# Performance work log

Hardware: AMD Instinct MI355X
Metric: run time of the kernel (lower is better)

The kernel has to match this reference:

```python
import jax, jax.numpy as jnp
from jax import lax
import numpy as np

# dims
N_DIA, DLEN = 48, 64            # 48 dialogues, 64 utterances each
N = N_DIA * DLEN                # total utterances = 3072
D = 512                         # n_dim (modal feature dim)
H = 512                         # nhidden
NL = 2                          # GCNII layers
NS = 2                          # n_speakers
ALPHA, LAMDA = 0.1, 0.5
PI = float(np.pi)
SCALE = 0.99999                 # acos clamp factor from original code


def setup_inputs() -> dict:
    key = jax.random.key(0)
    ks = jax.random.split(key, 8)
    a = jax.random.normal(ks[0], (N, D), jnp.float32)
    v = jax.random.normal(ks[1], (N, D), jnp.float32)
    l = jax.random.normal(ks[2], (N, D), jnp.float32)
    qmask = jax.random.uniform(ks[3], (DLEN, N_DIA, NS), jnp.float32)
    dia_len = np.full((N_DIA,), DLEN, dtype=np.int64)  # static segment lengths
    # learned params
    W_spk = 0.02 * jax.random.normal(ks[4], (NS, D), jnp.float32)      # speaker_embeddings
    W0 = jax.random.normal(ks[5], (D, H), jnp.float32) / np.sqrt(D)    # graph_net.fcs[0]
    b0 = jnp.zeros((H,), jnp.float32)
    Wg = jax.random.normal(ks[6], (NL, H, H), jnp.float32) / np.sqrt(H)  # GCNII conv weights
    return {"a": a, "v": v, "l": l, "qmask": qmask, "dia_len": dia_len,
            "W_spk": W_spk, "W0": W0, "b0": b0, "Wg": Wg}


def _angular_sim(cs):
    # 1 - acos(cs*0.99999)/pi, clipped for numerical safety of acos
    return 1.0 - jnp.arccos(jnp.clip(cs * SCALE, -SCALE, SCALE)) / PI


def _build_adj(feats, seg_mask):
    # feats: list of 3 arrays [N, D]; seg_mask: [N, N] same-dialogue block mask
    n = feats[0].shape[0]
    normed = [f * jax.lax.rsqrt(jnp.sum(f * f, axis=1, keepdims=True)) for f in feats]
    adj = jnp.zeros((3 * n, 3 * n), feats[0].dtype)
    ar = jnp.arange(n)
    for m in range(3):
        for nn_ in range(3):
            if m == nn_:
                # within-modality: block-diagonal (per dialogue) angular cosine similarity
                sim = _angular_sim(normed[m] @ normed[m].T) * seg_mask
                adj = adj.at[m * n:(m + 1) * n, nn_ * n:(nn_ + 1) * n].set(sim)
            else:
                # cross-modality: only diagonal (same utterance) entries
                cs = jnp.sum(normed[m] * normed[nn_], axis=1)
                adj = adj.at[m * n + ar, nn_ * n + ar].set(_angular_sim(cs))
    # symmetric degree normalization D^-1/2 A D^-1/2
    dinv = jax.lax.rsqrt(adj.sum(axis=1))
    return adj * dinv[:, None] * dinv[None, :]


def reference(a, v, l, qmask, dia_len, W_spk, W0, b0, Wg):
    dl = np.asarray(dia_len)
    nb = dl.shape[0]
    # node -> (position-in-dialogue, dialogue-id), static from dia_len
    dia_id = np.repeat(np.arange(nb), dl)
    pos = np.concatenate([np.arange(x) for x in dl])
    qflat = qmask[pos, dia_id]                 # [N, NS], matches torch.cat order
    spk_idx = jnp.argmax(qflat, axis=-1)       # [N]
    l = l + W_spk[spk_idx]                     # use_speaker=True, 'l' in modals

    seg = jnp.asarray(dia_id)
    seg_mask = (seg[:, None] == seg[None, :]).astype(a.dtype)  # [N, N]
    adj = _build_adj([a, v, l], seg_mask)      # [3N, 3N]

    x = jnp.concatenate([a, v, l], axis=0)     # [3N, D]
    # GCNII_lyc (eval mode: dropout is identity)
    h0 = jax.nn.relu(x @ W0 + b0)              # [3N, H]
    thetas = jnp.log(LAMDA / jnp.arange(1, NL + 1, dtype=x.dtype) + 1.0)

    def step(h, wt):
        W, theta = wt
        hi = adj @ h
        support = (1.0 - ALPHA) * hi + ALPHA * h0   # variant=False
        h = jax.nn.relu(theta * (support @ W) + (1.0 - theta) * support)
        return h, None

    h, _ = lax.scan(step, h0, (Wg, thetas))
    feat = jnp.concatenate([x, h], axis=-1)    # use_residue=True -> [3N, D+H]
    n = a.shape[0]
    # regroup per-utterance modal features: [N, 3*(D+H)]
    out = jnp.concatenate([feat[:n], feat[n:2 * n], feat[2 * n:3 * n]], axis=-1)
    return out
```

## Files before the change

kernel.cpp:

```cpp
#include <hip/hip_runtime.h>
#include <math.h>

#define N_DIA 48
#define NTOT  3072
#define DD    512
#define M3    9216
#define SEG   ((size_t)NTOT * DD)

#define SCALE_F 0.99999f
#define PI_F    3.14159274101257324f

typedef __attribute__((ext_vector_type(8))) short frag8;
typedef __attribute__((ext_vector_type(4))) float f32x4;

__device__ __forceinline__ float ang_sim(float cs) {
    float cc = cs * SCALE_F;
    cc = fminf(fmaxf(cc, -SCALE_F), SCALE_F);
    return 1.0f - acosf(cc) / PI_F;
}
__device__ __forceinline__ unsigned short f2bf(float x) {
    union { float f; unsigned int u; } c; c.f = x;
    unsigned int r = c.u + 0x7fffu + ((c.u >> 16) & 1u);
    return (unsigned short)(r >> 16);
}
__device__ __forceinline__ float bf2f(unsigned short h) {
    union { unsigned int u; float f; } c; c.u = ((unsigned int)h) << 16;
    return c.f;
}
__device__ __forceinline__ void gload16(const unsigned short* g, unsigned short* s) {
    __builtin_amdgcn_global_load_lds(
        (const __attribute__((address_space(1))) unsigned int*)g,
        (__attribute__((address_space(3))) unsigned int*)s, 16, 0, 0);
}

__global__ __launch_bounds__(256) void k_pre_wt(
    const float* __restrict__ a, const float* __restrict__ v,
    const float* __restrict__ l, const float* __restrict__ qmask,
    const float* __restrict__ Wspk, const float* __restrict__ W0,
    const float* __restrict__ Wg,
    float* __restrict__ out, unsigned short* __restrict__ xb,
    float* __restrict__ invn, float* __restrict__ cross,
    unsigned short* __restrict__ Wt)
{
    __shared__ float tile[32][33];
    int b = blockIdx.x;
    if (b < 768) {
        int wv = threadIdx.x >> 6, t = threadIdx.x & 63;
        int i = b * 4 + wv;
        int pos = i & 63, dia = i >> 6;
        int qb = (pos * N_DIA + dia) * 2;
        float q0 = qmask[qb], q1 = qmask[qb + 1];
        int spk = (q0 >= q1) ? 0 : 1;
        const float4* av4 = (const float4*)(a + (size_t)i * DD);
        const float4* vv4 = (const float4*)(v + (size_t)i * DD);
        const float4* lv4 = (const float4*)(l + (size_t)i * DD);
        const float4* wv4 = (const float4*)(Wspk + (size_t)spk * DD);
        float* ob = out + (size_t)i * 3072;
        float saa = 0, svv = 0, sll = 0, sav = 0, sal = 0, svl = 0;
#pragma unroll
        for (int e = 0; e < 2; e++) {
            int idx = e * 64 + t;
            float4 xa = av4[idx], xv = vv4[idx], xd = lv4[idx], xw = wv4[idx];
            float4 xL = make_float4(xd.x + xw.x, xd.y + xw.y, xd.z + xw.z, xd.w + xw.w);
            *(float4*)(ob + idx * 4)        = xa;
            *(float4*)(ob + 1024 + idx * 4) = xv;
            *(float4*)(ob + 2048 + idx * 4) = xL;
            ushort4 ya, yv, yl;
            ya.x = f2bf(xa.x); ya.y = f2bf(xa.y); ya.z = f2bf(xa.z); ya.w = f2bf(xa.w);
            yv.x = f2bf(xv.x); yv.y = f2bf(xv.y); yv.z = f2bf(xv.z); yv.w = f2bf(xv.w);
            yl.x = f2bf(xL.x); yl.y = f2bf(xL.y); yl.z = f2bf(xL.z); yl.w = f2bf(xL.w);
            *(ushort4*)(xb + (size_t)i * DD + idx * 4) = ya;
            *(ushort4*)(xb + SEG + (size_t)i * DD + idx * 4) = yv;
            *(ushort4*)(xb + 2 * SEG + (size_t)i * DD + idx * 4) = yl;
            saa += xa.x * xa.x + xa.y * xa.y + xa.z * xa.z + xa.w * xa.w;
            svv += xv.x * xv.x + xv.y * xv.y + xv.z * xv.z + xv.w * xv.w;
            sll += xL.x * xL.x + xL.y * xL.y + xL.z * xL.z + xL.w * xL.w;
            sav += xa.x * xv.x + xa.y * xv.y + xa.z * xv.z + xa.w * xv.w;
            sal += xa.x * xL.x + xa.y * xL.y + xa.z * xL.z + xa.w * xL.w;
            svl += xv.x * xL.x + xv.y * xL.y + xv.z * xL.z + xv.w * xL.w;
        }
#pragma unroll
        for (int off = 32; off; off >>= 1) {
            saa += __shfl_down(saa, off, 64);
            svv += __shfl_down(svv, off, 64);
            sll += __shfl_down(sll, off, 64);
            sav += __shfl_down(sav, off, 64);
            sal += __shfl_down(sal, off, 64);
            svl += __shfl_down(svl, off, 64);
        }
        if (t == 0) {
            float ina = 1.0f / sqrtf(saa);
            float inv_ = 1.0f / sqrtf(svv);
            float inl = 1.0f / sqrtf(sll);
            invn[i] = ina; invn[NTOT + i] = inv_; invn[2 * NTOT + i] = inl;
            cross[i]            = ang_sim(sav * ina * inv_);
            cross[NTOT + i]     = ang_sim(sal * ina * inl);
            cross[2 * NTOT + i] = ang_sim(svl * inv_ * inl);
        }
    } else {
        int idx = b - 768;
        int mm = idx >> 8;
        int by = (idx >> 4) & 15, bx = idx & 15;
        const float* W = (mm == 0) ? W0 : Wg + (size_t)(mm - 1) * DD * DD;
        int t = threadIdx.x, tx = t & 31, ty = t >> 5;
#pragma unroll
        for (int q = 0; q < 4; q++) {
            int k = by * 32 + ty + q * 8;
            tile[ty + q * 8][tx] = W[(size_t)k * DD + bx * 32 + tx];
        }
        __syncthreads();
#pragma unroll
        for (int q = 0; q < 4; q++) {
            int n = bx * 32 + ty + q * 8;
            Wt[(size_t)mm * DD * DD + (size_t)n * DD + by * 32 + tx] = f2bf(tile[tx][ty + q * 8]);
        }
    }
}

__global__ __launch_bounds__(256) void k_gram_mfma(
    const unsigned short* __restrict__ xb, const float* __restrict__ invn,
    const float* __restrict__ cross, float* __restrict__ blk,
    float* __restrict__ dinv)
{
    __shared__ __align__(16) unsigned short Xs[16 * 2048];
    int d = blockIdx.x, m = blockIdx.y;
    int t = threadIdx.x;
    int lane = t & 63, wv = t >> 6;
    int mrow = m * NTOT + d * 64;
    const unsigned short* src = xb + (size_t)mrow * DD;
    int sunit = ((t & 3) ^ ((t >> 2) & 3)) * 8;
#pragma unroll
    for (int c = 0; c < 16; c++) {
        gload16(src + (size_t)(t >> 2) * DD + c * 32 + sunit,
                &Xs[c * 2048 + wv * 512]);
    }
    __syncthreads();

    int rsel = lane & 15, quad = lane >> 4;
    int sq = (quad ^ (rsel & 3)) * 8;
    f32x4 acc[4];
#pragma unroll
    for (int j = 0; j < 4; j++) acc[j] = (f32x4){0.f, 0.f, 0.f, 0.f};
#pragma unroll
    for (int c = 0; c < 16; c++) {
        const unsigned short* base = &Xs[c * 2048];
        frag8 bf[4];
#pragma unroll
        for (int j = 0; j < 4; j++)
            bf[j] = *(const frag8*)&base[(j * 16 + rsel) * 32 + sq];
        frag8 af = *(const frag8*)&base[(wv * 16 + rsel) * 32 + sq];
#pragma unroll
        for (int j = 0; j < 4; j++)
            acc[j] = __builtin_amdgcn_mfma_f32_16x16x32_bf16(af, bf[j], acc[j], 0, 0, 0);
    }

    size_t bbase = (size_t)(m * N_DIA + d) * 4096;
    int rowl0 = wv * 16 + quad * 4;
    float ir[4], rs[4] = {0.f, 0.f, 0.f, 0.f};
#pragma unroll
    for (int r = 0; r < 4; r++) ir[r] = invn[mrow + rowl0 + r];
#pragma unroll
    for (int j = 0; j < 4; j++) {
        int coll = j * 16 + rsel;
        float ic = invn[mrow + coll];
#pragma unroll
        for (int r = 0; r < 4; r++) {
            float sim = ang_sim(acc[j][r] * ir[r] * ic);
            blk[bbase + (size_t)(rowl0 + r) * 64 + coll] = sim;
            rs[r] += sim;
        }
    }
#pragma unroll
    for (int off = 8; off; off >>= 1)
#pragma unroll
        for (int r = 0; r < 4; r++) rs[r] += __shfl_down(rs[r], off, 16);
    if (rsel == 0) {
#pragma unroll
        for (int r = 0; r < 4; r++) {
            int gi = d * 64 + rowl0 + r;
            float c1, c2;
            if (m == 0)      { c1 = cross[gi];        c2 = cross[NTOT + gi]; }
            else if (m == 1) { c1 = cross[gi];        c2 = cross[2 * NTOT + gi]; }
            else             { c1 = cross[NTOT + gi]; c2 = cross[2 * NTOT + gi]; }
            dinv[m * NTOT + gi] = 1.0f / sqrtf(rs[r] + c1 + c2);
        }
    }
}

__global__ __launch_bounds__(256) void k_gemm(
    const unsigned short* __restrict__ A, const unsigned short* __restrict__ W,
    const float* __restrict__ bias,
    unsigned short* __restrict__ oRows, unsigned short* __restrict__ oT,
    float theta, int mode,
    const unsigned short* __restrict__ A2, unsigned short* __restrict__ oRows2)
{
    __shared__ __align__(16) char smem[53248];
    unsigned short* const As0 = (unsigned short*)smem;
    unsigned short* const As1 = (unsigned short*)(smem + 4096);
    unsigned short* const Bs0 = (unsigned short*)(smem + 8192);
    unsigned short* const Bs1 = (unsigned short*)(smem + 16384);
    unsigned short* const tH  = (unsigned short*)smem;
    unsigned short* const tR  = (unsigned short*)(smem + 17408);
    unsigned short* const tT  = (unsigned short*)(smem + 34816);

    int t = threadIdx.x, lane = t & 63, wv = t >> 6;
    int bx = blockIdx.x, by = blockIdx.y;
    const unsigned short* Ap = A;
    unsigned short* oR = oRows;
    unsigned short* oTp = oT;
    if (by >= 144) { Ap = A2; oR = oRows2; oTp = nullptr; by -= 144; }
    int mbase = by * 64, nbase = bx * 128;
    int srow = lane >> 2;
    int scol = (((lane & 3) ^ (srow & 3)) * 8);
    int rsel = lane & 15, quad = lane >> 4;
    int sq = (quad ^ (rsel & 3)) * 8;

    const unsigned short* Ag  = Ap + (size_t)(mbase + wv * 16 + srow) * DD + scol;
    const unsigned short* Bg0 = W  + (size_t)(nbase + wv * 32 + srow) * DD + scol;
    const unsigned short* Bg1 = W  + (size_t)(nbase + wv * 32 + 16 + srow) * DD + scol;

    f32x4 acc[8];
#pragma unroll
    for (int i = 0; i < 8; i++) acc[i] = (f32x4){0.f, 0.f, 0.f, 0.f};

    gload16(Ag,  As0 + wv * 512);
    gload16(Bg0, Bs0 + wv * 1024);
    gload16(Bg1, Bs0 + wv * 1024 + 512);

#pragma unroll
    for (int kt = 0; kt < 16; kt++) {
        __syncthreads();
        const unsigned short* Ac = (kt & 1) ? As1 : As0;
        const unsigned short* Bc = (kt & 1) ? Bs1 : Bs0;
        if (kt < 15) {
            unsigned short* An = (kt & 1) ? As0 : As1;
            unsigned short* Bn = (kt & 1) ? Bs0 : Bs1;
            gload16(Ag + (kt + 1) * 32,  An + wv * 512);
            gload16(Bg0 + (kt + 1) * 32, Bn + wv * 1024);
            gload16(Bg1 + (kt + 1) * 32, Bn + wv * 1024 + 512);
        }
        frag8 af[4], bfr[2];
#pragma unroll
        for (int i = 0; i < 4; i++)
            af[i] = *(const frag8*)&Ac[(i * 16 + rsel) * 32 + sq];
#pragma unroll
        for (int j = 0; j < 2; j++)
            bfr[j] = *(const frag8*)&Bc[(wv * 32 + j * 16 + rsel) * 32 + sq];
#pragma unroll
        for (int i = 0; i < 4; i++)
#pragma unroll
            for (int j = 0; j < 2; j++)
                acc[i * 2 + j] = __builtin_amdgcn_mfma_f32_16x16x32_bf16(
                    af[i], bfr[j], acc[i * 2 + j], 0, 0, 0);
    }
    __syncthreads();

    int r = t >> 2, c0 = (t & 3) * 32;
    if (mode == 1) {
        const unsigned short* srcA = Ap + (size_t)(mbase + r) * DD + nbase + c0;
#pragma unroll
        for (int u = 0; u < 4; u++)
            *(uint4*)&tH[r * 136 + c0 + u * 8] = *(const uint4*)(srcA + u * 8);
        __syncthreads();
    }
    float omt = 1.0f - theta;
#pragma unroll
    for (int i = 0; i < 4; i++)
#pragma unroll
        for (int j = 0; j < 2; j++) {
            int cl = wv * 32 + j * 16 + rsel;
            float bv = 0.f;
            if (mode == 0) bv = bias[nbase + cl];
            float vv[4];
#pragma unroll
            for (int rr = 0; rr < 4; rr++) {
                int rl = i * 16 + quad * 4 + rr;
                float x = acc[i * 2 + j][rr];
                if (mode == 0) x = fmaxf(x + bv, 0.f);
                else           x = theta * x + omt * bf2f(tH[rl * 136 + cl]);
                vv[rr] = x;
            }
#pragma unroll
            for (int rr = 0; rr < 4; rr++)
                tR[(i * 16 + quad * 4 + rr) * 136 + cl] = f2bf(vv[rr]);
            if (oTp) {
                ushort4 w4;
                w4.x = f2bf(vv[0]); w4.y = f2bf(vv[1]);
                w4.z = f2bf(vv[2]); w4.w = f2bf(vv[3]);
                *(ushort4*)&tT[cl * 72 + i * 16 + quad * 4] = w4;
            }
        }
    __syncthreads();
    {
        unsigned short* dst = oR + (size_t)(mbase + r) * DD + nbase + c0;
#pragma unroll
        for (int u = 0; u < 4; u++)
            *(uint4*)(dst + u * 8) = *(const uint4*)&tR[r * 136 + c0 + u * 8];
    }
    if (oTp) {
        int c = t >> 1, r0 = (t & 1) * 32;
        unsigned short* dst = oTp + (size_t)(nbase + c) * M3 + mbase + r0;
#pragma unroll
        for (int u = 0; u < 4; u++)
            *(uint4*)(dst + u * 8) = *(const uint4*)&tT[c * 72 + r0 + u * 8];
    }
}

__global__ __launch_bounds__(256) void k_adj(
    const float* __restrict__ blk, const float* __restrict__ cross,
    const float* __restrict__ dinv,
    const unsigned short* __restrict__ GT, const unsigned short* __restrict__ Gr,
    const unsigned short* __restrict__ P0,
// ... 93 lines not shown
        }
    }
    if (!final_mode) {
        __syncthreads();
        int r = t >> 2, c0 = (t & 3) * 32;
        unsigned short* dst = hout + (size_t)(m * NTOT + dbase + r) * DD + cbase + c0;
#pragma unroll
        for (int u = 0; u < 4; u++)
            *(uint4*)(dst + u * 8) = *(const uint4*)&OT[r * 136 + c0 + u * 8];
    }
}

extern "C" void kernel_launch(void* const* d_in, const int* in_sizes, int n_in,
                              void* d_out, int out_size, void* d_ws, size_t ws_size,
                              hipStream_t stream) {
    (void)in_sizes; (void)n_in; (void)out_size; (void)ws_size;
    const float* a     = (const float*)d_in[0];
    const float* v     = (const float*)d_in[1];
    const float* l     = (const float*)d_in[2];
    const float* qmask = (const float*)d_in[3];
    const float* Wspk  = (const float*)d_in[5];
    const float* W0    = (const float*)d_in[6];
    const float* b0    = (const float*)d_in[7];
    const float* Wg    = (const float*)d_in[8];
    float* out = (float*)d_out;
    float* ws = (float*)d_ws;

    float* invn  = ws;
    float* blk   = invn + M3;
    float* cross = blk + (size_t)3 * N_DIA * 4096;
    float* dinvp = cross + M3;
    unsigned short* Wt  = (unsigned short*)(dinvp + M3);
    unsigned short* xb  = Wt + (size_t)3 * DD * DD;
    unsigned short* h0  = xb  + 3 * SEG;
    unsigned short* G1r = h0  + 3 * SEG;
    unsigned short* G1T = G1r + 3 * SEG;
    unsigned short* h1  = G1T + 3 * SEG;
    unsigned short* G2r = xb;
    unsigned short* G2T = G1r;
    unsigned short* P02 = G1T;

    const float th1 = 0.40546510810816438f;
    const float th2 = 0.22314355131420976f;

    k_pre_wt<<<1536, 256, 0, stream>>>(a, v, l, qmask, Wspk, W0, Wg, out, xb, invn, cross, Wt);
    k_gram_mfma<<<dim3(N_DIA, 3), 256, 0, stream>>>(xb, invn, cross, blk, dinvp);

    k_gemm<<<dim3(4, 144), 256, 0, stream>>>(xb, Wt, b0, h0, nullptr, 0.f, 0, nullptr, nullptr);
    k_gemm<<<dim3(4, 144), 256, 0, stream>>>(h0, Wt + (size_t)DD * DD, nullptr, G1r, G1T,
                                             th1, 1, nullptr, nullptr);
    k_adj<<<dim3(4, N_DIA, 3), 256, 0, stream>>>(blk, cross, dinvp, G1T, G1r, G1r,
                                                 h1, nullptr, 0);
    k_gemm<<<dim3(4, 288), 256, 0, stream>>>(h1, Wt + (size_t)2 * DD * DD, nullptr, G2r, G2T,
                                             th2, 1, h0, P02);
    k_adj<<<dim3(4, N_DIA, 3), 256, 0, stream>>>(blk, cross, dinvp, G2T, G2r, P02,
                                                 nullptr, out, 1);
}
```

Before: 199.7 us.

## Fuse preprocessing with gram kernel and chain h0, G1, P02 GEMMs in one kernel

```diff
diff --git a/kernel.cpp b/kernel.cpp
--- a/kernel.cpp
+++ b/kernel.cpp
@@ -32,53 +32,86 @@
         (const __attribute__((address_space(1))) unsigned int*)g,
         (__attribute__((address_space(3))) unsigned int*)s, 16, 0, 0);
 }
-
-__global__ __launch_bounds__(256) void k_pre_wt(
+__device__ __forceinline__ float d8(float4 x0, float4 x1, float4 y0, float4 y1) {
+    return x0.x*y0.x + x0.y*y0.y + x0.z*y0.z + x0.w*y0.w
+         + x1.x*y1.x + x1.y*y1.y + x1.z*y1.z + x1.w*y1.w;
+}
+
+__global__ __launch_bounds__(512) void k_pre_gram_wt(
     const float* __restrict__ a, const float* __restrict__ v,
     const float* __restrict__ l, const float* __restrict__ qmask,
     const float* __restrict__ Wspk, const float* __restrict__ W0,
     const float* __restrict__ Wg,
     float* __restrict__ out, unsigned short* __restrict__ xb,
-    float* __restrict__ invn, float* __restrict__ cross,
-    unsigned short* __restrict__ Wt)
+    float* __restrict__ cross, float* __restrict__ blk,
+    float* __restrict__ dinv, unsigned short* __restrict__ Wt)
 {
-    __shared__ float tile[32][33];
+    __shared__ __align__(16) char smem[66816];
     int b = blockIdx.x;
-    if (b < 768) {
-        int wv = threadIdx.x >> 6, t = threadIdx.x & 63;
-        int i = b * 4 + wv;
-        int pos = i & 63, dia = i >> 6;
-        int qb = (pos * N_DIA + dia) * 2;
+    int t = threadIdx.x;
+
+    if (b >= 144) {
+        float (*tile)[32][33] = (float (*)[32][33])smem;
+        int sub = t >> 8, tid = t & 255;
+        int idx = (b - 144) * 2 + sub;
+        int mm = idx >> 8, rem = idx & 255;
+        int by = rem >> 4, bx = rem & 15;
+        const float* W = (mm == 0) ? W0 : Wg + (size_t)(mm - 1) * DD * DD;
+        int tx = tid & 31, ty = tid >> 5;
+#pragma unroll
+        for (int q = 0; q < 4; q++) {
+            int k = by * 32 + ty + q * 8;
+            tile[sub][ty + q * 8][tx] = W[(size_t)k * DD + bx * 32 + tx];
+        }
+        __syncthreads();
+#pragma unroll
+        for (int q = 0; q < 4; q++) {
+            int n = bx * 32 + ty + q * 8;
+            Wt[(size_t)mm * DD * DD + (size_t)n * DD + by * 32 + tx] = f2bf(tile[sub][tx][ty + q * 8]);
+        }
+        return;
+    }
+
+    unsigned short* Xs = (unsigned short*)smem;
+    float* invnL = (float*)(smem + 65536);
+    float* c1L = invnL + 64;
+    float* c2L = c1L + 64;
+    int d = b % N_DIA, m = b / N_DIA;
+    int lane = t & 63, wv = t >> 6;
+    int dbase = d * 64;
+
+    for (int u = 0; u < 8; u++) {
+        int r = u * 8 + wv;
+        int i = dbase + r;
+        int qb = (r * N_DIA + d) * 2;
         float q0 = qmask[qb], q1 = qmask[qb + 1];
         int spk = (q0 >= q1) ? 0 : 1;
-        const float4* av4 = (const float4*)(a + (size_t)i * DD);
-        const float4* vv4 = (const float4*)(v + (size_t)i * DD);
-        const float4* lv4 = (const float4*)(l + (size_t)i * DD);
-        const float4* wv4 = (const float4*)(Wspk + (size_t)spk * DD);
-        float* ob = out + (size_t)i * 3072;
-        float saa = 0, svv = 0, sll = 0, sav = 0, sal = 0, svl = 0;
-#pragma unroll
-        for (int e = 0; e < 2; e++) {
-            int idx = e * 64 + t;
-            float4 xa = av4[idx], xv = vv4[idx], xd = lv4[idx], xw = wv4[idx];
-            float4 xL = make_float4(xd.x + xw.x, xd.y + xw.y, xd.z + xw.z, xd.w + xw.w);
-            *(float4*)(ob + idx * 4)        = xa;
-            *(float4*)(ob + 1024 + idx * 4) = xv;
-            *(float4*)(ob + 2048 + idx * 4) = xL;
-            ushort4 ya, yv, yl;
-            ya.x = f2bf(xa.x); ya.y = f2bf(xa.y); ya.z = f2bf(xa.z); ya.w = f2bf(xa.w);
-            yv.x = f2bf(xv.x); yv.y = f2bf(xv.y); yv.z = f2bf(xv.z); yv.w = f2bf(xv.w);
-            yl.x = f2bf(xL.x); yl.y = f2bf(xL.y); yl.z = f2bf(xL.z); yl.w = f2bf(xL.w);
-            *(ushort4*)(xb + (size_t)i * DD + idx * 4) = ya;
-            *(ushort4*)(xb + SEG + (size_t)i * DD + idx * 4) = yv;
-            *(ushort4*)(xb + 2 * SEG + (size_t)i * DD + idx * 4) = yl;
-            saa += xa.x * xa.x + xa.y * xa.y + xa.z * xa.z + xa.w * xa.w;
-            svv += xv.x * xv.x + xv.y * xv.y + xv.z * xv.z + xv.w * xv.w;
-            sll += xL.x * xL.x + xL.y * xL.y + xL.z * xL.z + xL.w * xL.w;
-            sav += xa.x * xv.x + xa.y * xv.y + xa.z * xv.z + xa.w * xv.w;
-            sal += xa.x * xL.x + xa.y * xL.y + xa.z * xL.z + xa.w * xL.w;
-            svl += xv.x * xL.x + xv.y * xL.y + xv.z * xL.z + xv.w * xL.w;
-        }
+        const float4* ap = (const float4*)(a + (size_t)i * DD) + lane * 2;
+        const float4* vp = (const float4*)(v + (size_t)i * DD) + lane * 2;
+        const float4* lp = (const float4*)(l + (size_t)i * DD) + lane * 2;
+        const float4* wp = (const float4*)(Wspk + (size_t)spk * DD) + lane * 2;
+        float4 a0 = ap[0], a1 = ap[1];
+        float4 v0 = vp[0], v1 = vp[1];
+        float4 l0 = lp[0], l1 = lp[1];
+        float4 w0 = wp[0], w1 = wp[1];
+        float4 L0 = make_float4(l0.x + w0.x, l0.y + w0.y, l0.z + w0.z, l0.w + w0.w);
+        float4 L1 = make_float4(l1.x + w1.x, l1.y + w1.y, l1.z + w1.z, l1.w + w1.w);
+        float* ob = out + (size_t)i * 3072 + m * 1024 + lane * 8;
+        if (m == 0)      { *(float4*)ob = a0; *(float4*)(ob + 4) = a1; }
+        else if (m == 1) { *(float4*)ob = v0; *(float4*)(ob + 4) = v1; }
+        else             { *(float4*)ob = L0; *(float4*)(ob + 4) = L1; }
+        float4 m0, m1;
+        if (m == 0) { m0 = a0; m1 = a1; } else if (m == 1) { m0 = v0; m1 = v1; }
+        else { m0 = L0; m1 = L1; }
+        ushort4 y0, y1;
+        y0.x = f2bf(m0.x); y0.y = f2bf(m0.y); y0.z = f2bf(m0.z); y0.w = f2bf(m0.w);
+        y1.x = f2bf(m1.x); y1.y = f2bf(m1.y); y1.z = f2bf(m1.z); y1.w = f2bf(m1.w);
+        unsigned short* xg = xb + (size_t)m * SEG + (size_t)i * DD + lane * 8;
+        *(ushort4*)xg = y0; *(ushort4*)(xg + 4) = y1;
+        unsigned short* xd = &Xs[(lane >> 2) * 2048 + r * 32 + (((lane & 3) ^ (r & 3)) << 3)];
+        *(ushort4*)xd = y0; *(ushort4*)(xd + 4) = y1;
+        float saa = d8(a0, a1, a0, a1), svv = d8(v0, v1, v0, v1), sll = d8(L0, L1, L0, L1);
+        float sav = d8(a0, a1, v0, v1), sal = d8(a0, a1, L0, L1), svl = d8(v0, v1, L0, L1);
 #pragma unroll
         for (int off = 32; off; off >>= 1) {
             saa += __shfl_down(saa, off, 64);
@@ -88,103 +121,289 @@
             sal += __shfl_down(sal, off, 64);
             svl += __shfl_down(svl, off, 64);
         }
-        if (t == 0) {
+        if (lane == 0) {
             float ina = 1.0f / sqrtf(saa);
             float inv_ = 1.0f / sqrtf(svv);
             float inl = 1.0f / sqrtf(sll);
-            invn[i] = ina; invn[NTOT + i] = inv_; invn[2 * NTOT + i] = inl;
-            cross[i]            = ang_sim(sav * ina * inv_);
-            cross[NTOT + i]     = ang_sim(sal * ina * inl);
-            cross[2 * NTOT + i] = ang_sim(svl * inv_ * inl);
-        }
-    } else {
-        int idx = b - 768;
-        int mm = idx >> 8;
-        int by = (idx >> 4) & 15, bx = idx & 15;
-        const float* W = (mm == 0) ? W0 : Wg + (size_t)(mm - 1) * DD * DD;
-        int t = threadIdx.x, tx = t & 31, ty = t >> 5;
-#pragma unroll
-        for (int q = 0; q < 4; q++) {
-            int k = by * 32 + ty + q * 8;
-            tile[ty + q * 8][tx] = W[(size_t)k * DD + bx * 32 + tx];
-        }
-        __syncthreads();
-#pragma unroll
-        for (int q = 0; q < 4; q++) {
-            int n = bx * 32 + ty + q * 8;
-            Wt[(size_t)mm * DD * DD + (size_t)n * DD + by * 32 + tx] = f2bf(tile[tx][ty + q * 8]);
-        }
-    }
-}
-
-__global__ __launch_bounds__(256) void k_gram_mfma(
-    const unsigned short* __restrict__ xb, const float* __restrict__ invn,
-    const float* __restrict__ cross, float* __restrict__ blk,
-    float* __restrict__ dinv)
+            float s_av = ang_sim(sav * ina * inv_);
+            float s_al = ang_sim(sal * ina * inl);
+            float s_vl = ang_sim(svl * inv_ * inl);
+            if (m == 0) { cross[i] = s_av; cross[NTOT + i] = s_al; cross[2 * NTOT + i] = s_vl; }
+            invnL[r] = (m == 0) ? ina : ((m == 1) ? inv_ : inl);
+            c1L[r] = (m == 2) ? s_al : s_av;
+            c2L[r] = (m == 0) ? s_al : s_vl;
+        }
+    }
+    __syncthreads();
+
+    if (wv < 4) {
+        int rsel = lane & 15, quad = lane >> 4;
+        int sq = (quad ^ (rsel & 3)) * 8;
+        f32x4 acc[4];
+#pragma unroll
+        for (int j = 0; j < 4; j++) acc[j] = (f32x4){0.f, 0.f, 0.f, 0.f};
+#pragma unroll
+        for (int c = 0; c < 16; c++) {
+            const unsigned short* base = &Xs[c * 2048];
+            frag8 bf[4];
+#pragma unroll
+            for (int j = 0; j < 4; j++)
+                bf[j] = *(const frag8*)&base[(j * 16 + rsel) * 32 + sq];
+            frag8 af = *(const frag8*)&base[(wv * 16 + rsel) * 32 + sq];
+#pragma unroll
+            for (int j = 0; j < 4; j++)
+                acc[j] = __builtin_amdgcn_mfma_f32_16x16x32_bf16(af, bf[j], acc[j], 0, 0, 0);
+        }
+        size_t bbase = (size_t)(m * N_DIA + d) * 4096;
+        int rowl0 = wv * 16 + quad * 4;
+        float ir[4], rs[4] = {0.f, 0.f, 0.f, 0.f};
+#pragma unroll
+        for (int r = 0; r < 4; r++) ir[r] = invnL[rowl0 + r];
+#pragma unroll
+        for (int j = 0; j < 4; j++) {
+            int coll = j * 16 + rsel;
+            float ic = invnL[coll];
+#pragma unroll
+            for (int r = 0; r < 4; r++) {
+                float sim = ang_sim(acc[j][r] * ir[r] * ic);
+                blk[bbase + (size_t)(rowl0 + r) * 64 + coll] = sim;
+                rs[r] += sim;
+            }
+        }
+#pragma unroll
+        for (int off = 8; off; off >>= 1)
+#pragma unroll
+            for (int r = 0; r < 4; r++) rs[r] += __shfl_down(rs[r], off, 16);
+        if (rsel == 0) {
+#pragma unroll
+            for (int r = 0; r < 4; r++) {
+                int rl = rowl0 + r;
+                dinv[m * NTOT + dbase + rl] = 1.0f / sqrtf(rs[r] + c1L[rl] + c2L[rl]);
+            }
+        }
+    }
+}
+
+__global__ __launch_bounds__(512) void k_fgemm(
+    const unsigned short* __restrict__ xb, const unsigned short* __restrict__ Wt,
+    const float* __restrict__ bias,
+    unsigned short* __restrict__ G1r, unsigned short* __restrict__ G1T,
+    unsigned short* __restrict__ P02, float th1, float th2)
 {
-    __shared__ __align__(16) unsigned short Xs[16 * 2048];
-    int d = blockIdx.x, m = blockIdx.y;
-    int t = threadIdx.x;
-    int lane = t & 63, wv = t >> 6;
-    int mrow = m * NTOT + d * 64;
-    const unsigned short* src = xb + (size_t)mrow * DD;
-    int sunit = ((t & 3) ^ ((t >> 2) & 3)) * 8;
-#pragma unroll
-    for (int c = 0; c < 16; c++) {
-        gload16(src + (size_t)(t >> 2) * DD + c * 32 + sunit,
-                &Xs[c * 2048 + wv * 512]);
-    }
-    __syncthreads();
-
+    __shared__ __align__(16) char smem[102400];
+    unsigned short* const Xs0 = (unsigned short*)smem;
+    unsigned short* const Xs1 = (unsigned short*)(smem + 2048);
+    unsigned short* const Bs0 = (unsigned short*)(smem + 4096);
+    unsigned short* const Bs1 = (unsigned short*)(smem + 36864);
+    unsigned short* const H0s = (unsigned short*)(smem + 69632);
+    unsigned short* const tS  = (unsigned short*)(smem + 4096);
+
+    int t = threadIdx.x, lane = t & 63, wv = t >> 6;
+    int mbase = blockIdx.x * 32;
+    int srow = lane >> 2;
+    int scol = ((lane & 3) ^ (srow & 3)) * 8;
     int rsel = lane & 15, quad = lane >> 4;
     int sq = (quad ^ (rsel & 3)) * 8;
-    f32x4 acc[4];
-#pragma unroll
-    for (int j = 0; j < 4; j++) acc[j] = (f32x4){0.f, 0.f, 0.f, 0.f};
-#pragma unroll
-    for (int c = 0; c < 16; c++) {
-        const unsigned short* base = &Xs[c * 2048];
-        frag8 bf[4];
+
+    const unsigned short* W0t = Wt;
+    const unsigned short* W1t = Wt + (size_t)DD * DD;
+    const unsigned short* W2t = Wt + (size_t)2 * DD * DD;
+    const unsigned short* Ag = xb + (size_t)(mbase + wv * 16 + srow) * DD + scol;
+
+    f32x4 acc[8];
+
+#define STAGE_B(Wb, kt, Bd) do { \
+    const unsigned short* _s = (Wb) + (size_t)(wv * 64 + srow) * DD + (kt) * 32 + scol; \
+    unsigned short* _d = (Bd) + (wv * 64) * 32; \
+    gload16(_s,                       _d); \
+    gload16(_s + (size_t)16 * DD,     _d + 512); \
+    gload16(_s + (size_t)32 * DD,     _d + 1024); \
+    gload16(_s + (size_t)48 * DD,     _d + 1536); \
+} while (0)
+
+#pragma unroll
+    for (int z = 0; z < 8; z++) acc[z] = (f32x4){0.f, 0.f, 0.f, 0.f};
+    if (wv < 2) gload16(Ag, Xs0 + wv * 512);
+    STAGE_B(W0t, 0, Bs0);
+    for (int kt = 0; kt < 16; kt++) {
+        __syncthreads();
+        const unsigned short* Xc = (kt & 1) ? Xs1 : Xs0;
+        const unsigned short* Bc = (kt & 1) ? Bs1 : Bs0;
+        if (kt < 15) {
+            unsigned short* Xn = (kt & 1) ? Xs0 : Xs1;
+            unsigned short* Bn = (kt & 1) ? Bs0 : Bs1;
+            if (wv < 2) gload16(Ag + (kt + 1) * 32, Xn + wv * 512);
+            STAGE_B(W0t, kt + 1, Bn);
+        }
+        frag8 af[2], bfr[4];
+#pragma unroll
+        for (int i = 0; i < 2; i++)
+            af[i] = *(const frag8*)&Xc[(i * 16 + rsel) * 32 + sq];
 #pragma unroll
         for (int j = 0; j < 4; j++)
-            bf[j] = *(const frag8*)&base[(j * 16 + rsel) * 32 + sq];
-        frag8 af = *(const frag8*)&base[(wv * 16 + rsel) * 32 + sq];
+            bfr[j] = *(const frag8*)&Bc[(wv * 64 + j * 16 + rsel) * 32 + sq];
+#pragma unroll
+        for (int i = 0; i < 2; i++)
+#pragma unroll
+            for (int j = 0; j < 4; j++)
+                acc[i * 4 + j] = __builtin_amdgcn_mfma_f32_16x16x32_bf16(
+                    af[i], bfr[j], acc[i * 4 + j], 0, 0, 0);
+    }
+#pragma unroll
+    for (int i = 0; i < 2; i++)
+#pragma unroll
+        for (int j = 0; j < 4; j++) {
+            int col = wv * 64 + j * 16 + rsel;
+            float bv = bias[col];
+#pragma unroll
+            for (int rr = 0; rr < 4; rr++) {
+                int row = i * 16 + quad * 4 + rr;
+                float x = fmaxf(acc[i * 4 + j][rr] + bv, 0.f);
+                H0s[row * 512 + (((col >> 3) ^ (row & 7)) << 3) + (col & 7)] = f2bf(x);
+            }
+        }
+
+#pragma unroll
+    for (int z = 0; z < 8; z++) acc[z] = (f32x4){0.f, 0.f, 0.f, 0.f};
+    STAGE_B(W1t, 0, Bs0);
+    for (int kt = 0; kt < 16; kt++) {
+        __syncthreads();
+        const unsigned short* Bc = (kt & 1) ? Bs1 : Bs0;
+        if (kt < 15) {
+            unsigned short* Bn = (kt & 1) ? Bs0 : Bs1;
+            STAGE_B(W1t, kt + 1, Bn);
+        }
+        frag8 af[2], bfr[4];
+#pragma unroll
+        for (int i = 0; i < 2; i++) {
+            int row = i * 16 + rsel;
+            int pu = (kt * 4 + quad) ^ (row & 7);
+            af[i] = *(const frag8*)&H0s[row * 512 + pu * 8];
+        }
 #pragma unroll
         for (int j = 0; j < 4; j++)
-            acc[j] = __builtin_amdgcn_mfma_f32_16x16x32_bf16(af, bf[j], acc[j], 0, 0, 0);
-    }
-
-    size_t bbase = (size_t)(m * N_DIA + d) * 4096;
-    int rowl0 = wv * 16 + quad * 4;
-    float ir[4], rs[4] = {0.f, 0.f, 0.f, 0.f};
-#pragma unroll
-    for (int r = 0; r < 4; r++) ir[r] = invn[mrow + rowl0 + r];
-#pragma unroll
-    for (int j = 0; j < 4; j++) {
-        int coll = j * 16 + rsel;
-        float ic = invn[mrow + coll];
-#pragma unroll
-        for (int r = 0; r < 4; r++) {
-            float sim = ang_sim(acc[j][r] * ir[r] * ic);
-            blk[bbase + (size_t)(rowl0 + r) * 64 + coll] = sim;
-            rs[r] += sim;
-        }
-    }
-#pragma unroll
-    for (int off = 8; off; off >>= 1)
-#pragma unroll
-        for (int r = 0; r < 4; r++) rs[r] += __shfl_down(rs[r], off, 16);
-    if (rsel == 0) {
-#pragma unroll
-        for (int r = 0; r < 4; r++) {
-            int gi = d * 64 + rowl0 + r;
-            float c1, c2;
-            if (m == 0)      { c1 = cross[gi];        c2 = cross[NTOT + gi]; }
-            else if (m == 1) { c1 = cross[gi];        c2 = cross[2 * NTOT + gi]; }
-            else             { c1 = cross[NTOT + gi]; c2 = cross[2 * NTOT + gi]; }
-            dinv[m * NTOT + gi] = 1.0f / sqrtf(rs[r] + c1 + c2);
-        }
-    }
+            bfr[j] = *(const frag8*)&Bc[(wv * 64 + j * 16 + rsel) * 32 + sq];
+#pragma unroll
+        for (int i = 0; i < 2; i++)
+#pragma unroll
+            for (int j = 0; j < 4; j++)
+                acc[i * 4 + j] = __builtin_amdgcn_mfma_f32_16x16x32_bf16(
+                    af[i], bfr[j], acc[i * 4 + j], 0, 0, 0);
+    }
+    {
+        float om1 = 1.0f - th1;
+#pragma unroll
+        for (int i = 0; i < 2; i++)
+#pragma unroll
+            for (int j = 0; j < 4; j++) {
+                int col = wv * 64 + j * 16 + rsel;
+#pragma unroll
+                for (int rr = 0; rr < 4; rr++) {
+                    int row = i * 16 + quad * 4 + rr;
+                    float h0v = bf2f(H0s[row * 512 + (((col >> 3) ^ (row & 7)) << 3) + (col & 7)]);
+                    acc[i * 4 + j][rr] = th1 * acc[i * 4 + j][rr] + om1 * h0v;
+                }
+            }
+    }
+    __syncthreads();
+#pragma unroll
+    for (int i = 0; i < 2; i++)
+#pragma unroll
+        for (int j = 0; j < 4; j++) {
+            int col = wv * 64 + j * 16 + rsel;
+#pragma unroll
+            for (int rr = 0; rr < 4; rr++)
+                tS[(i * 16 + quad * 4 + rr) * 520 + col] = f2bf(acc[i * 4 + j][rr]);
+        }
+    __syncthreads();
+    {
+        int rw = t >> 4, c0 = (t & 15) * 32;
+        unsigned short* dst = G1r + (size_t)(mbase + rw) * DD + c0;
+#pragma unroll
+        for (int u = 0; u < 4; u++)
+            *(uint4*)(dst + u * 8) = *(const uint4*)&tS[rw * 520 + c0 + u * 8];
+    }
+    __syncthreads();
+#pragma unroll
+    for (int i = 0; i < 2; i++)
+#pragma unroll
+        for (int j = 0; j < 4; j++) {
+            int col = wv * 64 + j * 16 + rsel;
+            ushort4 w4;
+            w4.x = f2bf(acc[i * 4 + j][0]); w4.y = f2bf(acc[i * 4 + j][1]);
+            w4.z = f2bf(acc[i * 4 + j][2]); w4.w = f2bf(acc[i * 4 + j][3]);
+            *(ushort4*)&tS[col * 40 + i * 16 + quad * 4] = w4;
+        }
+    __syncthreads();
+    {
+        unsigned short* dst = G1T + (size_t)t * M3 + mbase;
+#pragma unroll
+        for (int u = 0; u < 4; u++)
+            *(uint4*)(dst + u * 8) = *(const uint4*)&tS[t * 40 + u * 8];
+    }
+    __syncthreads();
+
+#pragma unroll
+    for (int z = 0; z < 8; z++) acc[z] = (f32x4){0.f, 0.f, 0.f, 0.f};
+    STAGE_B(W2t, 0, Bs0);
+    for (int kt = 0; kt < 16; kt++) {
+        __syncthreads();
+        const unsigned short* Bc = (kt & 1) ? Bs1 : Bs0;
+        if (kt < 15) {
+            unsigned short* Bn = (kt & 1) ? Bs0 : Bs1;
+            STAGE_B(W2t, kt + 1, Bn);
+        }
+        frag8 af[2], bfr[4];
+#pragma unroll
+        for (int i = 0; i < 2; i++) {
+            int row = i * 16 + rsel;
+            int pu = (kt * 4 + quad) ^ (row & 7);
+            af[i] = *(const frag8*)&H0s[row * 512 + pu * 8];
+        }
+#pragma unroll
+        for (int j = 0; j < 4; j++)
+            bfr[j] = *(const frag8*)&Bc[(wv * 64 + j * 16 + rsel) * 32 + sq];
+#pragma unroll
+        for (int i = 0; i < 2; i++)
+#pragma unroll
+            for (int j = 0; j < 4; j++)
+                acc[i * 4 + j] = __builtin_amdgcn_mfma_f32_16x16x32_bf16(
+                    af[i], bfr[j], acc[i * 4 + j], 0, 0, 0);
+    }
+    {
+        float om2 = 1.0f - th2;
+#pragma unroll
+        for (int i = 0; i < 2; i++)
+#pragma unroll
+            for (int j = 0; j < 4; j++) {
+                int col = wv * 64 + j * 16 + rsel;
+#pragma unroll
+                for (int rr = 0; rr < 4; rr++) {
+                    int row = i * 16 + quad * 4 + rr;
+                    float h0v = bf2f(H0s[row * 512 + (((col >> 3) ^ (row & 7)) << 3) + (col & 7)]);
+                    acc[i * 4 + j][rr] = th2 * acc[i * 4 + j][rr] + om2 * h0v;
+                }
+            }
+    }
+    __syncthreads();
+#pragma unroll
+    for (int i = 0; i < 2; i++)
+#pragma unroll
+        for (int j = 0; j < 4; j++) {
+            int col = wv * 64 + j * 16 + rsel;
+#pragma unroll
+            for (int rr = 0; rr < 4; rr++)
+                tS[(i * 16 + quad * 4 + rr) * 520 + col] = f2bf(acc[i * 4 + j][rr]);
+        }
+    __syncthreads();
+    {
+        int rw = t >> 4, c0 = (t & 15) * 32;
+        unsigned short* dst = P02 + (size_t)(mbase + rw) * DD + c0;
+#pragma unroll
+        for (int u = 0; u < 4; u++)
+            *(uint4*)(dst + u * 8) = *(const uint4*)&tS[rw * 520 + c0 + u * 8];
+    }
+#undef STAGE_B
 }
 
 __global__ __launch_bounds__(256) void k_gemm(
@@ -437,27 +656,23 @@
     float* dinvp = cross + M3;
     unsigned short* Wt  = (unsigned short*)(dinvp + M3);
     unsigned short* xb  = Wt + (size_t)3 * DD * DD;
-    unsigned short* h0  = xb  + 3 * SEG;
-    unsigned short* G1r = h0  + 3 * SEG;
+    unsigned short* P02 = xb  + 3 * SEG;
+    unsigned short* G1r = P02 + 3 * SEG;
     unsigned short* G1T = G1r + 3 * SEG;
     unsigned short* h1  = G1T + 3 * SEG;
     unsigned short* G2r = xb;
-    unsigned short* G2T = G1r;
-    unsigned short* P02 = G1T;
+    unsigned short* G2T = G1T;
 
     const float th1 = 0.40546510810816438f;
     const float th2 = 0.22314355131420976f;
 
-    k_pre_wt<<<1536, 256, 0, stream>>>(a, v, l, qmask, Wspk, W0, Wg, out, xb, invn, cross, Wt);
-    k_gram_mfma<<<dim3(N_DIA, 3), 256, 0, stream>>>(xb, invn, cross, blk, dinvp);
-
-    k_gemm<<<dim3(4, 144), 256, 0, stream>>>(xb, Wt, b0, h0, nullptr, 0.f, 0, nullptr, nullptr);
-    k_gemm<<<dim3(4, 144), 256, 0, stream>>>(h0, Wt + (size_t)DD * DD, nullptr, G1r, G1T,
-                                             th1, 1, nullptr, nullptr);
+    k_pre_gram_wt<<<528, 512, 0, stream>>>(a, v, l, qmask, Wspk, W0, Wg,
+                                           out, xb, cross, blk, dinvp, Wt);
+    k_fgemm<<<288, 512, 0, stream>>>(xb, Wt, b0, G1r, G1T, P02, th1, th2);
     k_adj<<<dim3(4, N_DIA, 3), 256, 0, stream>>>(blk, cross, dinvp, G1T, G1r, G1r,
                                                  h1, nullptr, 0);
-    k_gemm<<<dim3(4, 288), 256, 0, stream>>>(h1, Wt + (size_t)2 * DD * DD, nullptr, G2r, G2T,
-                                             th2, 1, h0, P02);
+    k_gemm<<<dim3(4, 144), 256, 0, stream>>>(h1, Wt + (size_t)2 * DD * DD, nullptr, G2r, G2T,
+                                             th2, 1, nullptr, nullptr);
     k_adj<<<dim3(4, N_DIA, 3), 256, 0, stream>>>(blk, cross, dinvp, G2T, G2r, P02,
                                                  nullptr, out, 1);
 }
```

Result: slower. 240.1 us (+20.3%).

## Fuse preprocessing with gram kernel and move h0·W2 GEMM earlier

Applied to the files above, without the earlier changes.

```diff
diff --git a/kernel.cpp b/kernel.cpp
--- a/kernel.cpp
+++ b/kernel.cpp
@@ -32,53 +32,86 @@
         (const __attribute__((address_space(1))) unsigned int*)g,
         (__attribute__((address_space(3))) unsigned int*)s, 16, 0, 0);
 }
-
-__global__ __launch_bounds__(256) void k_pre_wt(
+__device__ __forceinline__ float d8(float4 x0, float4 x1, float4 y0, float4 y1) {
+    return x0.x*y0.x + x0.y*y0.y + x0.z*y0.z + x0.w*y0.w
+         + x1.x*y1.x + x1.y*y1.y + x1.z*y1.z + x1.w*y1.w;
+}
+
+__global__ __launch_bounds__(512) void k_pre_gram_wt(
     const float* __restrict__ a, const float* __restrict__ v,
     const float* __restrict__ l, const float* __restrict__ qmask,
     const float* __restrict__ Wspk, const float* __restrict__ W0,
     const float* __restrict__ Wg,
     float* __restrict__ out, unsigned short* __restrict__ xb,
-    float* __restrict__ invn, float* __restrict__ cross,
-    unsigned short* __restrict__ Wt)
+    float* __restrict__ cross, float* __restrict__ blk,
+    float* __restrict__ dinv, unsigned short* __restrict__ Wt)
 {
-    __shared__ float tile[32][33];
+    __shared__ __align__(16) char smem[66816];
     int b = blockIdx.x;
-    if (b < 768) {
-        int wv = threadIdx.x >> 6, t = threadIdx.x & 63;
-        int i = b * 4 + wv;
-        int pos = i & 63, dia = i >> 6;
-        int qb = (pos * N_DIA + dia) * 2;
+    int t = threadIdx.x;
+
+    if (b >= 144) {
+        float (*tile)[32][33] = (float (*)[32][33])smem;
+        int sub = t >> 8, tid = t & 255;
+        int idx = (b - 144) * 2 + sub;
+        int mm = idx >> 8, rem = idx & 255;
+        int by = rem >> 4, bx = rem & 15;
+        const float* W = (mm == 0) ? W0 : Wg + (size_t)(mm - 1) * DD * DD;
+        int tx = tid & 31, ty = tid >> 5;
+#pragma unroll
+        for (int q = 0; q < 4; q++) {
+            int k = by * 32 + ty + q * 8;
+            tile[sub][ty + q * 8][tx] = W[(size_t)k * DD + bx * 32 + tx];
+        }
+        __syncthreads();
+#pragma unroll
+        for (int q = 0; q < 4; q++) {
+            int n = bx * 32 + ty + q * 8;
+            Wt[(size_t)mm * DD * DD + (size_t)n * DD + by * 32 + tx] = f2bf(tile[sub][tx][ty + q * 8]);
+        }
+        return;
+    }
+
+    unsigned short* Xs = (unsigned short*)smem;
+    float* invnL = (float*)(smem + 65536);
+    float* c1L = invnL + 64;
+    float* c2L = c1L + 64;
+    int d = b % N_DIA, m = b / N_DIA;
+    int lane = t & 63, wv = t >> 6;
+    int dbase = d * 64;
+
+    for (int u = 0; u < 8; u++) {
+        int r = u * 8 + wv;
+        int i = dbase + r;
+        int qb = (r * N_DIA + d) * 2;
         float q0 = qmask[qb], q1 = qmask[qb + 1];
         int spk = (q0 >= q1) ? 0 : 1;
-        const float4* av4 = (const float4*)(a + (size_t)i * DD);
-        const float4* vv4 = (const float4*)(v + (size_t)i * DD);
-        const float4* lv4 = (const float4*)(l + (size_t)i * DD);
-        const float4* wv4 = (const float4*)(Wspk + (size_t)spk * DD);
-        float* ob = out + (size_t)i * 3072;
-        float saa = 0, svv = 0, sll = 0, sav = 0, sal = 0, svl = 0;
-#pragma unroll
-        for (int e = 0; e < 2; e++) {
-            int idx = e * 64 + t;
-            float4 xa = av4[idx], xv = vv4[idx], xd = lv4[idx], xw = wv4[idx];
-            float4 xL = make_float4(xd.x + xw.x, xd.y + xw.y, xd.z + xw.z, xd.w + xw.w);
-            *(float4*)(ob + idx * 4)        = xa;
-            *(float4*)(ob + 1024 + idx * 4) = xv;
-            *(float4*)(ob + 2048 + idx * 4) = xL;
-            ushort4 ya, yv, yl;
-            ya.x = f2bf(xa.x); ya.y = f2bf(xa.y); ya.z = f2bf(xa.z); ya.w = f2bf(xa.w);
-            yv.x = f2bf(xv.x); yv.y = f2bf(xv.y); yv.z = f2bf(xv.z); yv.w = f2bf(xv.w);
-            yl.x = f2bf(xL.x); yl.y = f2bf(xL.y); yl.z = f2bf(xL.z); yl.w = f2bf(xL.w);
-            *(ushort4*)(xb + (size_t)i * DD + idx * 4) = ya;
-            *(ushort4*)(xb + SEG + (size_t)i * DD + idx * 4) = yv;
-            *(ushort4*)(xb + 2 * SEG + (size_t)i * DD + idx * 4) = yl;
-            saa += xa.x * xa.x + xa.y * xa.y + xa.z * xa.z + xa.w * xa.w;
-            svv += xv.x * xv.x + xv.y * xv.y + xv.z * xv.z + xv.w * xv.w;
-            sll += xL.x * xL.x + xL.y * xL.y + xL.z * xL.z + xL.w * xL.w;
-            sav += xa.x * xv.x + xa.y * xv.y + xa.z * xv.z + xa.w * xv.w;
-            sal += xa.x * xL.x + xa.y * xL.y + xa.z * xL.z + xa.w * xL.w;
-            svl += xv.x * xL.x + xv.y * xL.y + xv.z * xL.z + xv.w * xL.w;
-        }
+        const float4* ap = (const float4*)(a + (size_t)i * DD) + lane * 2;
+        const float4* vp = (const float4*)(v + (size_t)i * DD) + lane * 2;
+        const float4* lp = (const float4*)(l + (size_t)i * DD) + lane * 2;
+        const float4* wp = (const float4*)(Wspk + (size_t)spk * DD) + lane * 2;
+        float4 a0 = ap[0], a1 = ap[1];
+        float4 v0 = vp[0], v1 = vp[1];
+        float4 l0 = lp[0], l1 = lp[1];
+        float4 w0 = wp[0], w1 = wp[1];
+        float4 L0 = make_float4(l0.x + w0.x, l0.y + w0.y, l0.z + w0.z, l0.w + w0.w);
+        float4 L1 = make_float4(l1.x + w1.x, l1.y + w1.y, l1.z + w1.z, l1.w + w1.w);
+        float* ob = out + (size_t)i * 3072 + m * 1024 + lane * 8;
+        if (m == 0)      { *(float4*)ob = a0; *(float4*)(ob + 4) = a1; }
+        else if (m == 1) { *(float4*)ob = v0; *(float4*)(ob + 4) = v1; }
+        else             { *(float4*)ob = L0; *(float4*)(ob + 4) = L1; }
+        float4 m0, m1;
+        if (m == 0) { m0 = a0; m1 = a1; } else if (m == 1) { m0 = v0; m1 = v1; }
+        else { m0 = L0; m1 = L1; }
+        ushort4 y0, y1;
+        y0.x = f2bf(m0.x); y0.y = f2bf(m0.y); y0.z = f2bf(m0.z); y0.w = f2bf(m0.w);
+        y1.x = f2bf(m1.x); y1.y = f2bf(m1.y); y1.z = f2bf(m1.z); y1.w = f2bf(m1.w);
+        unsigned short* xg = xb + (size_t)m * SEG + (size_t)i * DD + lane * 8;
+        *(ushort4*)xg = y0; *(ushort4*)(xg + 4) = y1;
+        unsigned short* xd = &Xs[(lane >> 2) * 2048 + r * 32 + (((lane & 3) ^ (r & 3)) << 3)];
+        *(ushort4*)xd = y0; *(ushort4*)(xd + 4) = y1;
+        float saa = d8(a0, a1, a0, a1), svv = d8(v0, v1, v0, v1), sll = d8(L0, L1, L0, L1);
+        float sav = d8(a0, a1, v0, v1), sal = d8(a0, a1, L0, L1), svl = d8(v0, v1, L0, L1);
 #pragma unroll
         for (int off = 32; off; off >>= 1) {
             saa += __shfl_down(saa, off, 64);
@@ -88,101 +121,65 @@
             sal += __shfl_down(sal, off, 64);
             svl += __shfl_down(svl, off, 64);
         }
-        if (t == 0) {
+        if (lane == 0) {
             float ina = 1.0f / sqrtf(saa);
             float inv_ = 1.0f / sqrtf(svv);
             float inl = 1.0f / sqrtf(sll);
-            invn[i] = ina; invn[NTOT + i] = inv_; invn[2 * NTOT + i] = inl;
-            cross[i]            = ang_sim(sav * ina * inv_);
-            cross[NTOT + i]     = ang_sim(sal * ina * inl);
-            cross[2 * NTOT + i] = ang_sim(svl * inv_ * inl);
-        }
-    } else {
-        int idx = b - 768;
-        int mm = idx >> 8;
-        int by = (idx >> 4) & 15, bx = idx & 15;
-        const float* W = (mm == 0) ? W0 : Wg + (size_t)(mm - 1) * DD * DD;
-        int t = threadIdx.x, tx = t & 31, ty = t >> 5;
-#pragma unroll
-        for (int q = 0; q < 4; q++) {
-            int k = by * 32 + ty + q * 8;
-            tile[ty + q * 8][tx] = W[(size_t)k * DD + bx * 32 + tx];
-        }
-        __syncthreads();
-#pragma unroll
-        for (int q = 0; q < 4; q++) {
-            int n = bx * 32 + ty + q * 8;
-            Wt[(size_t)mm * DD * DD + (size_t)n * DD + by * 32 + tx] = f2bf(tile[tx][ty + q * 8]);
-        }
-    }
-}
-
-__global__ __launch_bounds__(256) void k_gram_mfma(
-    const unsigned short* __restrict__ xb, const float* __restrict__ invn,
-    const float* __restrict__ cross, float* __restrict__ blk,
-    float* __restrict__ dinv)
-{
-    __shared__ __align__(16) unsigned short Xs[16 * 2048];
-    int d = blockIdx.x, m = blockIdx.y;
-    int t = threadIdx.x;
-    int lane = t & 63, wv = t >> 6;
-    int mrow = m * NTOT + d * 64;
-    const unsigned short* src = xb + (size_t)mrow * DD;
-    int sunit = ((t & 3) ^ ((t >> 2) & 3)) * 8;
-#pragma unroll
-    for (int c = 0; c < 16; c++) {
-        gload16(src + (size_t)(t >> 2) * DD + c * 32 + sunit,
-                &Xs[c * 2048 + wv * 512]);
+            float s_av = ang_sim(sav * ina * inv_);
+            float s_al = ang_sim(sal * ina * inl);
+            float s_vl = ang_sim(svl * inv_ * inl);
+            if (m == 0) { cross[i] = s_av; cross[NTOT + i] = s_al; cross[2 * NTOT + i] = s_vl; }
+            invnL[r] = (m == 0) ? ina : ((m == 1) ? inv_ : inl);
+            c1L[r] = (m == 2) ? s_al : s_av;
+            c2L[r] = (m == 0) ? s_al : s_vl;
+        }
     }
     __syncthreads();
 
-    int rsel = lane & 15, quad = lane >> 4;
-    int sq = (quad ^ (rsel & 3)) * 8;
-    f32x4 acc[4];
-#pragma unroll
-    for (int j = 0; j < 4; j++) acc[j] = (f32x4){0.f, 0.f, 0.f, 0.f};
-#pragma unroll
-    for (int c = 0; c < 16; c++) {
-        const unsigned short* base = &Xs[c * 2048];
-        frag8 bf[4];
-#pragma unroll
-        for (int j = 0; j < 4; j++)
-            bf[j] = *(const frag8*)&base[(j * 16 + rsel) * 32 + sq];
-        frag8 af = *(const frag8*)&base[(wv * 16 + rsel) * 32 + sq];
-#pragma unroll
-        for (int j = 0; j < 4; j++)
-            acc[j] = __builtin_amdgcn_mfma_f32_16x16x32_bf16(af, bf[j], acc[j], 0, 0, 0);
-    }
-
-    size_t bbase = (size_t)(m * N_DIA + d) * 4096;
-    int rowl0 = wv * 16 + quad * 4;
-    float ir[4], rs[4] = {0.f, 0.f, 0.f, 0.f};
-#pragma unroll
-    for (int r = 0; r < 4; r++) ir[r] = invn[mrow + rowl0 + r];
-#pragma unroll
-    for (int j = 0; j < 4; j++) {
-        int coll = j * 16 + rsel;
-        float ic = invn[mrow + coll];
-#pragma unroll
-        for (int r = 0; r < 4; r++) {
-            float sim = ang_sim(acc[j][r] * ir[r] * ic);
-            blk[bbase + (size_t)(rowl0 + r) * 64 + coll] = sim;
-            rs[r] += sim;
-        }
-    }
-#pragma unroll
-    for (int off = 8; off; off >>= 1)
-#pragma unroll
-        for (int r = 0; r < 4; r++) rs[r] += __shfl_down(rs[r], off, 16);
-    if (rsel == 0) {
-#pragma unroll
-        for (int r = 0; r < 4; r++) {
-            int gi = d * 64 + rowl0 + r;
-            float c1, c2;
-            if (m == 0)      { c1 = cross[gi];        c2 = cross[NTOT + gi]; }
-            else if (m == 1) { c1 = cross[gi];        c2 = cross[2 * NTOT + gi]; }
-            else             { c1 = cross[NTOT + gi]; c2 = cross[2 * NTOT + gi]; }
-            dinv[m * NTOT + gi] = 1.0f / sqrtf(rs[r] + c1 + c2);
+    if (wv < 4) {
+        int rsel = lane & 15, quad = lane >> 4;
+        int sq = (quad ^ (rsel & 3)) * 8;
+        f32x4 acc[4];
+#pragma unroll
+        for (int j = 0; j < 4; j++) acc[j] = (f32x4){0.f, 0.f, 0.f, 0.f};
+#pragma unroll
+        for (int c = 0; c < 16; c++) {
+            const unsigned short* base = &Xs[c * 2048];
+            frag8 bf[4];
+#pragma unroll
+            for (int j = 0; j < 4; j++)
+                bf[j] = *(const frag8*)&base[(j * 16 + rsel) * 32 + sq];
+            frag8 af = *(const frag8*)&base[(wv * 16 + rsel) * 32 + sq];
+#pragma unroll
+            for (int j = 0; j < 4; j++)
+                acc[j] = __builtin_amdgcn_mfma_f32_16x16x32_bf16(af, bf[j], acc[j], 0, 0, 0);
+        }
+        size_t bbase = (size_t)(m * N_DIA + d) * 4096;
+        int rowl0 = wv * 16 + quad * 4;
+        float ir[4], rs[4] = {0.f, 0.f, 0.f, 0.f};
+#pragma unroll
+        for (int r = 0; r < 4; r++) ir[r] = invnL[rowl0 + r];
+#pragma unroll
+        for (int j = 0; j < 4; j++) {
+            int coll = j * 16 + rsel;
+            float ic = invnL[coll];
+#pragma unroll
+            for (int r = 0; r < 4; r++) {
+                float sim = ang_sim(acc[j][r] * ir[r] * ic);
+                blk[bbase + (size_t)(rowl0 + r) * 64 + coll] = sim;
+                rs[r] += sim;
+            }
+        }
+#pragma unroll
+        for (int off = 8; off; off >>= 1)
+#pragma unroll
+            for (int r = 0; r < 4; r++) rs[r] += __shfl_down(rs[r], off, 16);
+        if (rsel == 0) {
+#pragma unroll
+            for (int r = 0; r < 4; r++) {
+                int rl = rowl0 + r;
+                dinv[m * NTOT + dbase + rl] = 1.0f / sqrtf(rs[r] + c1L[rl] + c2L[rl]);
+            }
         }
     }
 }
@@ -192,7 +189,8 @@
     const float* __restrict__ bias,
     unsigned short* __restrict__ oRows, unsigned short* __restrict__ oT,
     float theta, int mode,
-    const unsigned short* __restrict__ A2, unsigned short* __restrict__ oRows2)
+    const unsigned short* __restrict__ A2, unsigned short* __restrict__ oRows2,
+    const unsigned short* __restrict__ Wb, float thetab)
 {
     __shared__ __align__(16) char smem[53248];
     unsigned short* const As0 = (unsigned short*)smem;
@@ -206,9 +204,11 @@
     int t = threadIdx.x, lane = t & 63, wv = t >> 6;
     int bx = blockIdx.x, by = blockIdx.y;
     const unsigned short* Ap = A;
+    const unsigned short* Wp = W;
+    float th = theta;
     unsigned short* oR = oRows;
     unsigned short* oTp = oT;
-    if (by >= 144) { Ap = A2; oR = oRows2; oTp = nullptr; by -= 144; }
+    if (by >= 144) { Ap = A2; oR = oRows2; oTp = nullptr; Wp = Wb; th = thetab; by -= 144; }
     int mbase = by * 64, nbase = bx * 128;
     int srow = lane >> 2;
     int scol = (((lane & 3) ^ (srow & 3)) * 8);
@@ -216,8 +216,8 @@
     int sq = (quad ^ (rsel & 3)) * 8;
 
     const unsigned short* Ag  = Ap + (size_t)(mbase + wv * 16 + srow) * DD + scol;
-    const unsigned short* Bg0 = W  + (size_t)(nbase + wv * 32 + srow) * DD + scol;
-    const unsigned short* Bg1 = W  + (size_t)(nbase + wv * 32 + 16 + srow) * DD + scol;
+    const unsigned short* Bg0 = Wp + (size_t)(nbase + wv * 32 + srow) * DD + scol;
+    const unsigned short* Bg1 = Wp + (size_t)(nbase + wv * 32 + 16 + srow) * DD + scol;
 
     f32x4 acc[8];
 #pragma unroll
@@ -263,7 +263,7 @@
             *(uint4*)&tH[r * 136 + c0 + u * 8] = *(const uint4*)(srcA + u * 8);
         __syncthreads();
     }
-    float omt = 1.0f - theta;
+    float omt = 1.0f - th;
 #pragma unroll
     for (int i = 0; i < 4; i++)
 #pragma unroll
@@ -277,7 +277,7 @@
                 int rl = i * 16 + quad * 4 + rr;
                 float x = acc[i * 2 + j][rr];
                 if (mode == 0) x = fmaxf(x + bv, 0.f);
-                else           x = theta * x + omt * bf2f(tH[rl * 136 + cl]);
+                else           x = th * x + omt * bf2f(tH[rl * 136 + cl]);
                 vv[rr] = x;
             }
 #pragma unroll
@@ -441,23 +441,25 @@
     unsigned short* G1r = h0  + 3 * SEG;
     unsigned short* G1T = G1r + 3 * SEG;
     unsigned short* h1  = G1T + 3 * SEG;
-    unsigned short* G2r = xb;
-    unsigned short* G2T = G1r;
-    unsigned short* P02 = G1T;
+    unsigned short* P02 = xb;
+    unsigned short* G2r = G1r;
+    unsigned short* G2T = G1T;
 
     const float th1 = 0.40546510810816438f;
     const float th2 = 0.22314355131420976f;
-
-    k_pre_wt<<<1536, 256, 0, stream>>>(a, v, l, qmask, Wspk, W0, Wg, out, xb, invn, cross, Wt);
-    k_gram_mfma<<<dim3(N_DIA, 3), 256, 0, stream>>>(xb, invn, cross, blk, dinvp);
-
-    k_gemm<<<dim3(4, 144), 256, 0, stream>>>(xb, Wt, b0, h0, nullptr, 0.f, 0, nullptr, nullptr);
-    k_gemm<<<dim3(4, 144), 256, 0, stream>>>(h0, Wt + (size_t)DD * DD, nullptr, G1r, G1T,
-                                             th1, 1, nullptr, nullptr);
+    const unsigned short* Wt1 = Wt + (size_t)DD * DD;
+    const unsigned short* Wt2 = Wt + (size_t)2 * DD * DD;
+
+    k_pre_gram_wt<<<528, 512, 0, stream>>>(a, v, l, qmask, Wspk, W0, Wg,
+                                           out, xb, cross, blk, dinvp, Wt);
+    k_gemm<<<dim3(4, 144), 256, 0, stream>>>(xb, Wt, b0, h0, nullptr, 0.f, 0,
+                                             nullptr, nullptr, nullptr, 0.f);
+    k_gemm<<<dim3(4, 288), 256, 0, stream>>>(h0, Wt1, nullptr, G1r, G1T, th1, 1,
+                                             h0, P02, Wt2, th2);
     k_adj<<<dim3(4, N_DIA, 3), 256, 0, stream>>>(blk, cross, dinvp, G1T, G1r, G1r,
                                                  h1, nullptr, 0);
-    k_gemm<<<dim3(4, 288), 256, 0, stream>>>(h1, Wt + (size_t)2 * DD * DD, nullptr, G2r, G2T,
-                                             th2, 1, h0, P02);
+    k_gemm<<<dim3(4, 144), 256, 0, stream>>>(h1, Wt2, nullptr, G2r, G2T, th2, 1,
+                                             nullptr, nullptr, nullptr, 0.f);
     k_adj<<<dim3(4, N_DIA, 3), 256, 0, stream>>>(blk, cross, dinvp, G2T, G2r, P02,
                                                  nullptr, out, 1);
 }
```

After: 208.5 us. 1.04x slower.
